# Kernel optimization log

Hardware: AMD Instinct MI355X
Metric: run time of the kernel (lower is better)

## Reference

```python
import jax, jax.numpy as jnp
import numpy as np

RC = 4.6  # cutoff radius (Angstrom), from init_kwargs
FACTOR = 7.199822675975224  # constants.half_Hartree * constants.Bohr (eV*A)


def exp_cutoff(d, rc):
    # smooth exponential (bump) cutoff: exp(1 - 1/(1-(d/rc)^2)) for d<rc, else 0
    x = d / rc
    inside = x < 1.0
    xs = jnp.where(inside, x, 0.5)  # safe value to avoid nan in masked branch
    f = jnp.exp(1.0 - 1.0 / (1.0 - xs * xs))
    return jnp.where(inside, f, 0.0)


def setup_inputs() -> dict:
    key = jax.random.key(0)
    k1, k2 = jax.random.split(key)
    B, N = 64, 512
    # atoms in a 40 A box -> realistic long-range distances
    coord = jax.random.uniform(k1, (B, N, 3), dtype=jnp.float32) * 40.0
    charges = jax.random.normal(k2, (B, N), dtype=jnp.float32) * 0.3
    mask = jnp.ones((B, N), dtype=bool)  # all atoms valid (no padding)
    return {"coord": coord, "charges": charges, "mask": mask}


def reference(coord, charges, mask):
    # coul_simple: e = factor * sum_ij (1 - fc(d_ij)) * q_i * q_j / d_ij, per molecule
    B, N, _ = coord.shape
    pair_mask = mask[:, :, None] & mask[:, None, :]
    eye = jnp.eye(N, dtype=bool)[None]
    valid = pair_mask & ~eye  # mask self-pairs and padding (mask_ij_)
    disp = coord[:, :, None, :] - coord[:, None, :, :]          # [B,N,N,3]
    d2 = jnp.sum(disp * disp, axis=-1)                          # [B,N,N]
    d = jnp.sqrt(jnp.where(valid, d2, 1.0))                     # safe sqrt on diag
    fc = 1.0 - exp_cutoff(d, RC)
    qq = charges[:, :, None] * charges[:, None, :]              # q_i * q_j
    e_ij = jnp.where(valid, fc * qq / d, 0.0)
    return FACTOR * jnp.sum(e_ij, axis=(1, 2))                  # mol_sum -> [B]
```

## Files before the change

### kernel.cpp

```cpp
#include <hip/hip_runtime.h>

#define N_ATOMS 512
#define JSPLIT  8
#define JLEN    (N_ATOMS / JSPLIT)
#define BLOCK   512
#define FACTOR  7.199822675975224f
#define RC2     (4.6f * 4.6f)

__global__ __launch_bounds__(BLOCK) void coul_pair_kernel(
    const float* __restrict__ coord,
    const float* __restrict__ charges,
    float* __restrict__ partials)
{
    const int b = blockIdx.x >> 3;
    const int s = blockIdx.x & 7;

    __shared__ float4 atom[N_ATOMS];

    const float* c = coord   + (size_t)b * N_ATOMS * 3;
    const float* q = charges + (size_t)b * N_ATOMS;
    const int t = threadIdx.x;
    atom[t] = make_float4(c[3 * t], c[3 * t + 1], c[3 * t + 2], q[t]);
    __syncthreads();

    const int i = t;
    const float4 ai = atom[i];
    const float inv_rc2 = 1.0f / RC2;
    const float4* __restrict__ base = &atom[s * JLEN];

    float acc = 0.0f;
    #pragma unroll 8
    for (int k = 0; k < JLEN; ++k) {
        const float4 aj = base[k];
        float dx = ai.x - aj.x, dy = ai.y - aj.y, dz = ai.z - aj.z;
        float d2 = dx * dx + dy * dy + dz * dz;
        float term = aj.w * rsqrtf(d2);
        if (d2 < RC2)
            term *= (1.0f - __expf(1.0f - 1.0f / (1.0f - d2 * inv_rc2)));
        acc += (s * JLEN + k == i) ? 0.0f : term;
    }
    acc *= ai.w;

    #pragma unroll
    for (int off = 32; off > 0; off >>= 1)
        acc += __shfl_down(acc, off, 64);

    __shared__ float wsum[BLOCK / 64];
    if ((t & 63) == 0) wsum[t >> 6] = acc;
    __syncthreads();
    if (t == 0) {
        float sum = 0.0f;
        #pragma unroll
        for (int w = 0; w < BLOCK / 64; ++w) sum += wsum[w];
        partials[blockIdx.x] = sum;
    }
}

__global__ void coul_reduce_kernel(const float* __restrict__ partials,
                                   float* __restrict__ out, int B)
{
    const int b = threadIdx.x;
    if (b < B) {
        float sum = 0.0f;
        #pragma unroll
        for (int s = 0; s < JSPLIT; ++s) sum += partials[b * JSPLIT + s];
        out[b] = FACTOR * sum;
    }
}

extern "C" void kernel_launch(void* const* d_in, const int* in_sizes, int n_in,
                              void* d_out, int out_size, void* d_ws, size_t ws_size,
                              hipStream_t stream) {
    const float* coord   = (const float*)d_in[0];
    const float* charges = (const float*)d_in[1];
    float* out      = (float*)d_out;
    float* partials = (float*)d_ws;

    const int B = (n_in > 2 && in_sizes[1] != in_sizes[2])
                      ? in_sizes[1] / (N_ATOMS * 4)
                      : in_sizes[1] / N_ATOMS;

    coul_pair_kernel<<<B * JSPLIT, BLOCK, 0, stream>>>(coord, charges, partials);
    coul_reduce_kernel<<<1, 64, 0, stream>>>(partials, out, B);
}
```

Measured before the change: 73.42 us.

## Exploit pair symmetry with circulant tile schedule and simplify cutoff math

Restructures each block to process one 64-atom i-tile against four forward j-tiles plus half the diagonal tile, so each unordered pair is computed about once and the total is doubled at the end. The halfway tile is weighted by 0.5 to avoid double counting. The cutoff exponent is rewritten as exp(-d2/(rc2-d2)) using hardware rcp/rsq builtins, removing a divide. It trades some load imbalance and reduced precision of approximate reciprocals for roughly 40% fewer pair evaluations.

Measured after the change: 65.49 us. 10.8% less time.

```diff
diff --git a/kernel.cpp b/kernel.cpp
--- a/kernel.cpp
+++ b/kernel.cpp
@@ -1,11 +1,10 @@
 #include <hip/hip_runtime.h>
 
 #define N_ATOMS 512
-#define JSPLIT  8
-#define JLEN    (N_ATOMS / JSPLIT)
-#define BLOCK   512
+#define NTILE   8
+#define BLOCK   256
 #define FACTOR  7.199822675975224f
-#define RC2     (4.6f * 4.6f)
+#define RC2f    (4.6f * 4.6f)
 
 __global__ __launch_bounds__(BLOCK) void coul_pair_kernel(
     const float* __restrict__ coord,
@@ -13,32 +12,61 @@
     float* __restrict__ partials)
 {
     const int b = blockIdx.x >> 3;
-    const int s = blockIdx.x & 7;
+    const int c = blockIdx.x & 7;
 
     __shared__ float4 atom[N_ATOMS];
 
-    const float* c = coord   + (size_t)b * N_ATOMS * 3;
-    const float* q = charges + (size_t)b * N_ATOMS;
-    const int t = threadIdx.x;
-    atom[t] = make_float4(c[3 * t], c[3 * t + 1], c[3 * t + 2], q[t]);
+    const float* co = coord   + (size_t)b * N_ATOMS * 3;
+    const float* q  = charges + (size_t)b * N_ATOMS;
+    for (int k = threadIdx.x; k < N_ATOMS; k += BLOCK)
+        atom[k] = make_float4(co[3 * k], co[3 * k + 1], co[3 * k + 2], q[k]);
     __syncthreads();
 
-    const int i = t;
-    const float4 ai = atom[i];
-    const float inv_rc2 = 1.0f / RC2;
-    const float4* __restrict__ base = &atom[s * JLEN];
+    const int t    = threadIdx.x;
+    const int w    = t >> 6;
+    const int lane = t & 63;
+    const float4 ai = atom[(c << 6) + lane];
 
-    float acc = 0.0f;
-    #pragma unroll 8
-    for (int k = 0; k < JLEN; ++k) {
-        const float4 aj = base[k];
-        float dx = ai.x - aj.x, dy = ai.y - aj.y, dz = ai.z - aj.z;
-        float d2 = dx * dx + dy * dy + dz * dz;
-        float term = aj.w * rsqrtf(d2);
-        if (d2 < RC2)
-            term *= (1.0f - __expf(1.0f - 1.0f / (1.0f - d2 * inv_rc2)));
-        acc += (s * JLEN + k == i) ? 0.0f : term;
+    float accM = 0.0f;
+    float accS = 0.0f;
+
+    {
+        const float4* __restrict__ base = &atom[((c + w + 1) & 7) << 6];
+        #pragma unroll 8
+        for (int k = 0; k < 64; ++k) {
+            const float4 aj = base[k];
+            float dx = ai.x - aj.x, dy = ai.y - aj.y, dz = ai.z - aj.z;
+            float d2 = dx * dx + dy * dy + dz * dz;
+            float r  = __builtin_amdgcn_rsqf(d2);
+            float tv = aj.w * r;
+            accM += tv;
+            if (d2 < RC2f) {
+                float uu = __builtin_amdgcn_rcpf(RC2f - d2);
+                float e  = __expf(-d2 * uu);
+                accM -= tv * e;
+            }
+        }
     }
+    {
+        const int kk0 = w << 4;
+        const float4* __restrict__ base = &atom[(c << 6) + kk0];
+        #pragma unroll
+        for (int k = 0; k < 16; ++k) {
+            const float4 aj = base[k];
+            float dx = ai.x - aj.x, dy = ai.y - aj.y, dz = ai.z - aj.z;
+            float d2 = dx * dx + dy * dy + dz * dz;
+            float r  = __builtin_amdgcn_rsqf(d2);
+            float tv = (kk0 + k == lane) ? 0.0f : aj.w * r;
+            accS += tv;
+            if (d2 < RC2f) {
+                float uu = __builtin_amdgcn_rcpf(RC2f - d2);
+                float e  = __expf(-d2 * uu);
+                accS -= tv * e;
+            }
+        }
+    }
+
+    float acc = ((w == 3) ? 0.5f * accM : accM) + 0.5f * accS;
     acc *= ai.w;
 
     #pragma unroll
@@ -48,12 +76,8 @@
     __shared__ float wsum[BLOCK / 64];
     if ((t & 63) == 0) wsum[t >> 6] = acc;
     __syncthreads();
-    if (t == 0) {
-        float sum = 0.0f;
-        #pragma unroll
-        for (int w = 0; w < BLOCK / 64; ++w) sum += wsum[w];
-        partials[blockIdx.x] = sum;
-    }
+    if (t == 0)
+        partials[blockIdx.x] = wsum[0] + wsum[1] + wsum[2] + wsum[3];
 }
 
 __global__ void coul_reduce_kernel(const float* __restrict__ partials,
@@ -63,8 +87,8 @@
     if (b < B) {
         float sum = 0.0f;
         #pragma unroll
-        for (int s = 0; s < JSPLIT; ++s) sum += partials[b * JSPLIT + s];
-        out[b] = FACTOR * sum;
+        for (int s = 0; s < NTILE; ++s) sum += partials[b * NTILE + s];
+        out[b] = 2.0f * FACTOR * sum;
     }
 }
 
@@ -80,6 +104,6 @@
                       ? in_sizes[1] / (N_ATOMS * 4)
                       : in_sizes[1] / N_ATOMS;
 
-    coul_pair_kernel<<<B * JSPLIT, BLOCK, 0, stream>>>(coord, charges, partials);
+    coul_pair_kernel<<<B * NTILE, BLOCK, 0, stream>>>(coord, charges, partials);
     coul_reduce_kernel<<<1, 64, 0, stream>>>(partials, out, B);
 }
```
